# Performance work log

Hardware: AMD Instinct MI355X
Metric: run time of the kernel (lower is better)

## Reference

```python
import jax, jax.numpy as jnp
import numpy as np

K = 3
TAPS = K * K
STD = float(np.sqrt(2.0)) / K  # FilterNorm scale: relu gain / kernel_size


def filter_norm(f, axis):
    # torch FilterNorm: subtract mean, divide by unbiased std (+1e-10), scale by STD
    m = jnp.mean(f, axis=axis, keepdims=True)
    sd = jnp.std(f, axis=axis, keepdims=True, ddof=1)
    return (f - m) / (sd + 1e-10) * STD


def setup_inputs() -> dict:
    key = jax.random.key(0)
    ks = jax.random.split(key, 9)
    B, C, H, W = 4, 64, 192, 192
    mid = int(C * 0.2)  # se_ratio=0.2 -> 12
    f = lambda k, shape, s: jax.random.normal(k, shape, jnp.float32) * s
    return {
        'x':   f(ks[0], (B, C, H, W), 1.0),
        'sw':  f(ks[1], (TAPS, C), 0.05),        # spatial branch 1x1 conv weight
        'sb':  f(ks[2], (TAPS,), 0.05),
        'cw1': f(ks[3], (mid, C), 0.05),         # channel branch squeeze
        'cb1': f(ks[4], (mid,), 0.05),
        'cw2': f(ks[5], (C * TAPS, mid), 0.05),  # channel branch expand
        'cb2': f(ks[6], (C * TAPS,), 0.05),
        'w2':  f(ks[7], (C, C, 1, 9), 0.05),     # trailing 1x9 conv
        'b2':  f(ks[8], (C,), 0.05),
    }


def block_forward(x, sw, sb, cw1, cb1, cw2, cb2, w2, b2):
    B, C, H, W = x.shape
    # --- DDFPack ---
    # spatial filters: 1x1 conv -> (B, 9, H, W), FilterNorm across the 9 taps
    s = jnp.einsum('bchw,tc->bthw', x, sw) + sb[None, :, None, None]
    s = filter_norm(s, axis=1)
    # channel filters: GAP -> 1x1 -> relu -> 1x1 -> (B, C, 9), FilterNorm over taps
    g = x.mean(axis=(2, 3))                         # (B, C)
    h1 = jax.nn.relu(g @ cw1.T + cb1)               # (B, mid)
    cf = (h1 @ cw2.T + cb2).reshape(B, C, TAPS)     # (B, C, 9)
    cf = filter_norm(cf, axis=2)
    # decoupled dynamic filter apply: per-pixel depthwise 3x3, combine='mul', pad=1
    xp = jnp.pad(x, ((0, 0), (0, 0), (1, 1), (1, 1)))
    out = jnp.zeros_like(x)
    for idx in range(TAPS):  # fixed 9-tap loop, no big unfold intermediate
        i, j = idx // K, idx % K
        out = out + xp[:, :, i:i + H, j:j + W] * s[:, idx:idx + 1] * cf[:, :, idx, None, None]
    # --- LeakyReLU(0.1) -> 1x9 conv (pad (0,4)) -> residual add (res_scale=1) ---
    a = jnp.where(out >= 0, out, 0.1 * out)
    y = jax.lax.conv_general_dilated(a, w2, (1, 1), ((0, 0), (4, 4)),
                                     dimension_numbers=('NCHW', 'OIHW', 'NCHW'))
    y = y + b2[None, :, None, None]
    return x + y


def reference(x, sw, sb, cw1, cb1, cw2, cb2, w2, b2):
    return block_forward(x, sw, sb, cw1, cb1, cw2, cb2, w2, b2)
```

## Files before the change

kernel.cpp:

```cpp
#include <hip/hip_runtime.h>
#include <hip/hip_bf16.h>

#define B_    4
#define C_    64
#define H_    192
#define W_    192
#define TAPS_ 9
#define MID_  12
#define HW_   (H_ * W_)
#define K_TOT 576
#define AT_STRIDE 72
#define AT_ROWS   200

constexpr float STD_ = 0.47140452079103173f;

using bf16 = __hip_bfloat16;
typedef __attribute__((ext_vector_type(4))) float  f32x4;
typedef __attribute__((ext_vector_type(8))) short  short8;

__device__ __forceinline__ unsigned short f2bf_bits(float v) {
    union { bf16 h; unsigned short u; } cv;
    cv.h = __float2bfloat16(v);
    return cv.u;
}

__global__ __launch_bounds__(256) void k_prep(const float* __restrict__ w2,
                                              unsigned short* __restrict__ w2bf) {
    int d = blockIdx.x * 256 + threadIdx.x;
    int o = d / K_TOT;
    int rem = d - o * K_TOT;
    int t = rem >> 6;
    int c = rem & 63;
    float v = w2[(o * C_ + c) * TAPS_ + t];
    w2bf[d] = f2bf_bits(v);
}

__global__ __launch_bounds__(256) void k_mean(const float* __restrict__ x,
                                              float* __restrict__ partials) {
    int bx = blockIdx.x;
    int bc = bx / 3, part = bx - 3 * (bx / 3);
    const float4* p = (const float4*)(x + (size_t)bc * HW_ + part * 12288);
    float s = 0.f;
    #pragma unroll
    for (int k = 0; k < 12; ++k) {
        float4 u = p[threadIdx.x + k * 256];
        s += u.x + u.y + u.z + u.w;
    }
    #pragma unroll
    for (int off = 32; off; off >>= 1) s += __shfl_down(s, off);
    __shared__ float red[4];
    if ((threadIdx.x & 63) == 0) red[threadIdx.x >> 6] = s;
    __syncthreads();
    if (threadIdx.x == 0)
        partials[bx] = red[0] + red[1] + red[2] + red[3];
}

__global__ __launch_bounds__(256) void k_cf(const float* __restrict__ partials,
                                            const float* __restrict__ cw1,
                                            const float* __restrict__ cb1,
                                            const float* __restrict__ cw2,
                                            const float* __restrict__ cb2,
                                            float* __restrict__ cfn) {
    __shared__ float g_l[B_ * C_];
    __shared__ float h1_l[B_ * MID_];
    int tid = threadIdx.x;
    g_l[tid] = (partials[tid * 3] + partials[tid * 3 + 1] + partials[tid * 3 + 2])
               * (1.0f / HW_);
    __syncthreads();
    if (tid < B_ * MID_) {
        int b = tid / MID_, m = tid % MID_;
        float acc = cb1[m];
        for (int c = 0; c < C_; ++c) acc += g_l[b * C_ + c] * cw1[m * C_ + c];
        h1_l[tid] = fmaxf(acc, 0.f);
    }
    __syncthreads();
    int b = tid >> 6, c = tid & 63;
    float f[TAPS_];
    float mean = 0.f;
    #pragma unroll
    for (int t = 0; t < TAPS_; ++t) {
        int n = c * TAPS_ + t;
        float acc = cb2[n];
        #pragma unroll
        for (int m = 0; m < MID_; ++m) acc += h1_l[b * MID_ + m] * cw2[n * MID_ + m];
        f[t] = acc;
        mean += acc;
    }
    mean *= (1.f / TAPS_);
    float var = 0.f;
    #pragma unroll
    for (int t = 0; t < TAPS_; ++t) { float d = f[t] - mean; var += d * d; }
    var *= (1.f / (TAPS_ - 1));
    float scale = STD_ / (sqrtf(fmaxf(var, 0.f)) + 1e-10f);
    #pragma unroll
    for (int t = 0; t < TAPS_; ++t)
        cfn[(b * C_ + c) * TAPS_ + t] = (f[t] - mean) * scale;
}

__global__ __launch_bounds__(256, 4) void k_main(const float* __restrict__ x,
                                                 const float* __restrict__ sw,
                                                 const float* __restrict__ sb,
                                                 const float* __restrict__ cfn,
                                                 const unsigned short* __restrict__ w2bf,
                                                 const float* __restrict__ bias2,
                                                 float* __restrict__ out) {
    __shared__ __align__(16) char smem[38336];
    short*          aT   = (short*)smem;
    unsigned short* aT16 = (unsigned short*)smem;
    unsigned*       aT32 = (unsigned*)smem;
    float*          sw_l = (float*)smem;
    float*          s_l  = (float*)(smem + 28800);
    float*          cf_l = (float*)(smem + 35712);
    float*          b2_l = (float*)(smem + 38016);
    float*          sb_l = (float*)(smem + 38272);

    int bh = blockIdx.x;
    int bb = bh / H_;
    int h  = bh - bb * H_;
    int tid = threadIdx.x;

    for (int i = tid; i < TAPS_ * C_; i += 256) sw_l[i] = sw[i];
    for (int i = tid; i < C_ * TAPS_; i += 256) cf_l[i] = cfn[bb * C_ * TAPS_ + i];
    if (tid < C_) b2_l[tid] = bias2[tid];
    if (tid < TAPS_) sb_l[tid] = sb[tid];
    __syncthreads();

    if (tid < W_) {
        int w = tid;
        float acc[TAPS_];
        #pragma unroll
        for (int t = 0; t < TAPS_; ++t) acc[t] = sb_l[t];
        const float* px = x + (size_t)bb * C_ * HW_ + h * W_ + w;
        #pragma unroll 4
        for (int c = 0; c < C_; ++c) {
            float xv = px[(size_t)c * HW_];
            #pragma unroll
            for (int t = 0; t < TAPS_; ++t) acc[t] = fmaf(xv, sw_l[t * C_ + c], acc[t]);
        }
        float mean = 0.f;
        #pragma unroll
        for (int t = 0; t < TAPS_; ++t) mean += acc[t];
        mean *= (1.f / TAPS_);
        float var = 0.f;
        #pragma unroll
        for (int t = 0; t < TAPS_; ++t) { float d = acc[t] - mean; var += d * d; }
        var *= (1.f / (TAPS_ - 1));
        float scale = STD_ / (sqrtf(fmaxf(var, 0.f)) + 1e-10f);
        #pragma unroll
        for (int t = 0; t < TAPS_; ++t) s_l[t * W_ + w] = (acc[t] - mean) * scale;
    }
    __syncthreads();

    for (int i = tid; i < 8 * (AT_STRIDE / 2); i += 256) {
        int rowIdx = i / (AT_STRIDE / 2);
        int col    = i - rowIdx * (AT_STRIDE / 2);
        int r = (rowIdx < 4) ? rowIdx : (192 + rowIdx);
        aT32[r * (AT_STRIDE / 2) + col] = 0u;
    }

    {
        size_t bbase = (size_t)bb * C_ * HW_;
        int vm = (h - 1 >= 0), vp = (h + 1 < H_);
        #pragma unroll 1
        for (int k = 0; k < 48; ++k) {
            int p = tid + k * 256;
            int c = p / W_;
            int w = p - c * W_;
            const float* xc = x + bbase + (size_t)c * HW_ + (size_t)h * W_;
            float acc = 0.f;
            #pragma unroll
            for (int t = 0; t < TAPS_; ++t) {
                int r = t / 3, dc = t % 3;
                int ww = w - 1 + dc;
                int rok = (r == 0) ? vm : (r == 2) ? vp : 1;
                float xv = (rok && ww >= 0 && ww < W_)
                               ? xc[(r - 1) * W_ + ww] : 0.f;
                acc = fmaf(xv * s_l[t * W_ + w], cf_l[c * TAPS_ + t], acc);
            }
            acc = (acc >= 0.f) ? acc : 0.1f * acc;
            aT16[(w + 4) * AT_STRIDE + c] = f2bf_bits(acc);
        }
    }
    __syncthreads();

    {
        int lane = tid & 63, wid = tid >> 6;
        int quad = lane >> 4, l16 = lane & 15;
        int obase = wid * 16;

        f32x4 acc[12];
        #pragma unroll
        for (int n = 0; n < 12; ++n) acc[n] = (f32x4){0.f, 0.f, 0.f, 0.f};

        const short* w2s = (const short*)w2bf;
        const short* arow = w2s + (obase + l16) * K_TOT + quad * 8;

        #pragma unroll 2
        for (int kk = 0; kk < 18; ++kk) {
            short8 af = *(const short8*)(arow + kk * 32);
            int t = kk >> 1;
            int cstart = ((kk & 1) << 5) + (quad << 3);
            const short* bb8 = aT + (l16 + t) * AT_STRIDE + cstart;
            #pragma unroll
            for (int n = 0; n < 12; ++n) {
                short8 bf = *(const short8*)(bb8 + n * 16 * AT_STRIDE);
                acc[n] = __builtin_amdgcn_mfma_f32_16x16x32_bf16(af, bf, acc[n], 0, 0, 0);
            }
        }

        size_t xbase = (size_t)bb * C_ * HW_ + (size_t)h * W_;
        #pragma unroll
        for (int n = 0; n < 12; ++n) {
            int w = n * 16 + l16;
            #pragma unroll
            for (int reg = 0; reg < 4; ++reg) {
                int o = obase + quad * 4 + reg;
                size_t idx = xbase + (size_t)o * HW_ + w;
                out[idx] = acc[n][reg] + b2_l[o] + x[idx];
            }
        }
    }
}

extern "C" void kernel_launch(void* const* d_in, const int* in_sizes, int n_in,
                              void* d_out, int out_size, void* d_ws, size_t ws_size,
                              hipStream_t stream) {
    const float* x   = (const float*)d_in[0];
    const float* sw  = (const float*)d_in[1];
    const float* sb  = (const float*)d_in[2];
    const float* cw1 = (const float*)d_in[3];
    const float* cb1 = (const float*)d_in[4];
    const float* cw2 = (const float*)d_in[5];
    const float* cb2 = (const float*)d_in[6];
    const float* w2  = (const float*)d_in[7];
    const float* b2  = (const float*)d_in[8];
    float* out = (float*)d_out;

    unsigned short* w2bf = (unsigned short*)d_ws;
    float* partials = (float*)((char*)d_ws + 73728);
    float* cfn      = (float*)((char*)d_ws + 76800);

    hipLaunchKernelGGL(k_prep, dim3(144), dim3(256), 0, stream, w2, w2bf);
    hipLaunchKernelGGL(k_mean, dim3(768), dim3(256), 0, stream, x, partials);
    hipLaunchKernelGGL(k_cf, dim3(1), dim3(256), 0, stream,
                       partials, cw1, cb1, cw2, cb2, cfn);
    hipLaunchKernelGGL(k_main, dim3(B_ * H_), dim3(256), 0, stream,
                       x, sw, sb, cfn, w2bf, b2, out);
}
```

Measured before the change: 159.1 us.

## Register-block dynamic filter apply, fuse prep kernels, prefetch MFMA weights

```diff
diff --git a/kernel.cpp b/kernel.cpp
--- a/kernel.cpp
+++ b/kernel.cpp
@@ -10,7 +10,6 @@
 #define HW_   (H_ * W_)
 #define K_TOT 576
 #define AT_STRIDE 72
-#define AT_ROWS   200
 
 constexpr float STD_ = 0.47140452079103173f;
 
@@ -24,20 +23,21 @@
     return cv.u;
 }
 
-__global__ __launch_bounds__(256) void k_prep(const float* __restrict__ w2,
-                                              unsigned short* __restrict__ w2bf) {
-    int d = blockIdx.x * 256 + threadIdx.x;
-    int o = d / K_TOT;
-    int rem = d - o * K_TOT;
-    int t = rem >> 6;
-    int c = rem & 63;
-    float v = w2[(o * C_ + c) * TAPS_ + t];
-    w2bf[d] = f2bf_bits(v);
-}
-
-__global__ __launch_bounds__(256) void k_mean(const float* __restrict__ x,
-                                              float* __restrict__ partials) {
+__global__ __launch_bounds__(256) void k_pre(const float* __restrict__ x,
+                                             const float* __restrict__ w2,
+                                             unsigned short* __restrict__ w2bf,
+                                             float* __restrict__ partials) {
     int bx = blockIdx.x;
+    if (bx < 144) {
+        int d = bx * 256 + threadIdx.x;
+        int o = d / K_TOT;
+        int rem = d - o * K_TOT;
+        int t = rem >> 6;
+        int c = rem & 63;
+        w2bf[d] = f2bf_bits(w2[(o * C_ + c) * TAPS_ + t]);
+        return;
+    }
+    bx -= 144;
     int bc = bx / 3, part = bx - 3 * (bx / 3);
     const float4* p = (const float4*)(x + (size_t)bc * HW_ + part * 12288);
     float s = 0.f;
@@ -104,13 +104,11 @@
                                                  const unsigned short* __restrict__ w2bf,
                                                  const float* __restrict__ bias2,
                                                  float* __restrict__ out) {
-    __shared__ __align__(16) char smem[38336];
+    __shared__ __align__(16) char smem[38320];
     short*          aT   = (short*)smem;
-    unsigned short* aT16 = (unsigned short*)smem;
     unsigned*       aT32 = (unsigned*)smem;
     float*          sw_l = (float*)smem;
     float*          s_l  = (float*)(smem + 28800);
-    float*          cf_l = (float*)(smem + 35712);
     float*          b2_l = (float*)(smem + 38016);
     float*          sb_l = (float*)(smem + 38272);
 
@@ -120,7 +118,6 @@
     int tid = threadIdx.x;
 
     for (int i = tid; i < TAPS_ * C_; i += 256) sw_l[i] = sw[i];
-    for (int i = tid; i < C_ * TAPS_; i += 256) cf_l[i] = cfn[bb * C_ * TAPS_ + i];
     if (tid < C_) b2_l[tid] = bias2[tid];
     if (tid < TAPS_) sb_l[tid] = sb[tid];
     __syncthreads();
@@ -146,8 +143,9 @@
         for (int t = 0; t < TAPS_; ++t) { float d = acc[t] - mean; var += d * d; }
         var *= (1.f / (TAPS_ - 1));
         float scale = STD_ / (sqrtf(fmaxf(var, 0.f)) + 1e-10f);
-        #pragma unroll
-        for (int t = 0; t < TAPS_; ++t) s_l[t * W_ + w] = (acc[t] - mean) * scale;
+        float* sp = s_l + w * 12;
+        #pragma unroll
+        for (int t = 0; t < TAPS_; ++t) sp[t] = (acc[t] - mean) * scale;
     }
     __syncthreads();
 
@@ -159,26 +157,66 @@
     }
 
     {
-        size_t bbase = (size_t)bb * C_ * HW_;
-        int vm = (h - 1 >= 0), vp = (h + 1 < H_);
-        #pragma unroll 1
-        for (int k = 0; k < 48; ++k) {
-            int p = tid + k * 256;
-            int c = p / W_;
-            int w = p - c * W_;
-            const float* xc = x + bbase + (size_t)c * HW_ + (size_t)h * W_;
-            float acc = 0.f;
-            #pragma unroll
-            for (int t = 0; t < TAPS_; ++t) {
-                int r = t / 3, dc = t % 3;
-                int ww = w - 1 + dc;
-                int rok = (r == 0) ? vm : (r == 2) ? vp : 1;
-                float xv = (rok && ww >= 0 && ww < W_)
-                               ? xc[(r - 1) * W_ + ww] : 0.f;
-                acc = fmaf(xv * s_l[t * W_ + w], cf_l[c * TAPS_ + t], acc);
-            }
-            acc = (acc >= 0.f) ? acc : 0.1f * acc;
-            aT16[(w + 4) * AT_STRIDE + c] = f2bf_bits(acc);
+        int lane = tid & 63, wid = tid >> 6;
+        int wbase = wid * 16;
+        if (lane < 48) {
+            int w0 = 4 * lane;
+            float sreg[4][TAPS_];
+            #pragma unroll
+            for (int k = 0; k < 4; ++k) {
+                const float* sp = s_l + (w0 + k) * 12;
+                #pragma unroll
+                for (int t = 0; t < TAPS_; ++t) sreg[k][t] = sp[t];
+            }
+            bool l0 = (lane == 0), l47 = (lane == 47);
+            int rok0 = (h > 0), rok2 = (h < H_ - 1);
+            int midx = l0 ? 0 : (w0 - 1);
+            int pidx = l47 ? w0 : (w0 + 4);
+            const float* xbase = x + (long)bb * C_ * HW_ + (long)(h - 1) * W_;
+            #pragma unroll 1
+            for (int i = 0; i < 16; i += 2) {
+                int c0 = wbase + i;
+                int cu = __builtin_amdgcn_readfirstlane(c0);
+                const float* cfp = cfn + bb * (C_ * TAPS_) + cu * TAPS_;
+                const float* pc0 = xbase + (long)c0 * HW_;
+                const float* pc1 = pc0 + HW_;
+                float acc0[4] = {0.f, 0.f, 0.f, 0.f};
+                float acc1[4] = {0.f, 0.f, 0.f, 0.f};
+                #pragma unroll
+                for (int r = 0; r < 3; ++r) {
+                    if (r == 0 && !rok0) continue;
+                    if (r == 2 && !rok2) continue;
+                    const float* p0 = pc0 + r * W_;
+                    const float* p1 = pc1 + r * W_;
+                    float4 fa = *(const float4*)(p0 + w0);
+                    float4 fb = *(const float4*)(p1 + w0);
+                    float ma = l0 ? 0.f : p0[midx];
+                    float mb = l0 ? 0.f : p1[midx];
+                    float pa = l47 ? 0.f : p0[pidx];
+                    float pb = l47 ? 0.f : p1[pidx];
+                    float va[6] = { ma, fa.x, fa.y, fa.z, fa.w, pa };
+                    float vb[6] = { mb, fb.x, fb.y, fb.z, fb.w, pb };
+                    #pragma unroll
+                    for (int dc = 0; dc < 3; ++dc) {
+                        int t = r * 3 + dc;
+                        float cva = cfp[t];
+                        float cvb = cfp[TAPS_ + t];
+                        #pragma unroll
+                        for (int k = 0; k < 4; ++k) {
+                            acc0[k] = fmaf(va[k + dc] * sreg[k][t], cva, acc0[k]);
+                            acc1[k] = fmaf(vb[k + dc] * sreg[k][t], cvb, acc1[k]);
+                        }
+                    }
+                }
+                #pragma unroll
+                for (int k = 0; k < 4; ++k) {
+                    float a0 = acc0[k]; a0 = (a0 >= 0.f) ? a0 : 0.1f * a0;
+                    float a1 = acc1[k]; a1 = (a1 >= 0.f) ? a1 : 0.1f * a1;
+                    unsigned pk = (unsigned)f2bf_bits(a0)
+                                | ((unsigned)f2bf_bits(a1) << 16);
+                    aT32[(w0 + k + 4) * (AT_STRIDE / 2) + (c0 >> 1)] = pk;
+                }
+            }
         }
     }
     __syncthreads();
@@ -195,9 +233,11 @@
         const short* w2s = (const short*)w2bf;
         const short* arow = w2s + (obase + l16) * K_TOT + quad * 8;
 
-        #pragma unroll 2
+        short8 af = *(const short8*)(arow);
+        #pragma unroll 1
         for (int kk = 0; kk < 18; ++kk) {
-            short8 af = *(const short8*)(arow + kk * 32);
+            short8 afn = af;
+            if (kk < 17) afn = *(const short8*)(arow + (kk + 1) * 32);
             int t = kk >> 1;
             int cstart = ((kk & 1) << 5) + (quad << 3);
             const short* bb8 = aT + (l16 + t) * AT_STRIDE + cstart;
@@ -206,6 +246,7 @@
                 short8 bf = *(const short8*)(bb8 + n * 16 * AT_STRIDE);
                 acc[n] = __builtin_amdgcn_mfma_f32_16x16x32_bf16(af, bf, acc[n], 0, 0, 0);
             }
+            af = afn;
         }
 
         size_t xbase = (size_t)bb * C_ * HW_ + (size_t)h * W_;
@@ -240,8 +281,7 @@
     float* partials = (float*)((char*)d_ws + 73728);
     float* cfn      = (float*)((char*)d_ws + 76800);
 
-    hipLaunchKernelGGL(k_prep, dim3(144), dim3(256), 0, stream, w2, w2bf);
-    hipLaunchKernelGGL(k_mean, dim3(768), dim3(256), 0, stream, x, partials);
+    hipLaunchKernelGGL(k_pre, dim3(912), dim3(256), 0, stream, x, w2, w2bf, partials);
     hipLaunchKernelGGL(k_cf, dim3(1), dim3(256), 0, stream,
                        partials, cw1, cb1, cw2, cb2, cfn);
     hipLaunchKernelGGL(k_main, dim3(B_ * H_), dim3(256), 0, stream,
```

Result: faster. 149.6 us (-6.0%).
